# Kernel tuning notes

Hardware: AMD Instinct MI355X
Metric: run time of the kernel (lower is better)

Reference implementation:

```python
import jax, jax.numpy as jnp
import numpy as np

NUM_BINS = 16
D_MODEL = 128
TAIL_BOUND = 20.0
MIN_BIN_WIDTH = 1e-3
MIN_BIN_HEIGHT = 1e-3
MIN_DERIVATIVE = 1e-3
EPS = 1e-6


def setup_inputs() -> dict:
    key = jax.random.key(0)
    ks = jax.random.split(key, 10)
    B, S = 32, 8192
    sc = 0.05  # small init scale so spline logits stay moderate
    return {
        "inputs": jax.random.normal(ks[0], (B, S), dtype=jnp.float32),
        "conditioning": jax.random.normal(ks[1], (B, S, D_MODEL), dtype=jnp.float32),
        "Ww": jax.random.normal(ks[2], (NUM_BINS, D_MODEL), dtype=jnp.float32) * sc,
        "bw": jax.random.normal(ks[3], (NUM_BINS,), dtype=jnp.float32) * sc,
        "Wh": jax.random.normal(ks[4], (NUM_BINS, D_MODEL), dtype=jnp.float32) * sc,
        "bh": jax.random.normal(ks[5], (NUM_BINS,), dtype=jnp.float32) * sc,
        "Wd": jax.random.normal(ks[6], (NUM_BINS - 1, D_MODEL), dtype=jnp.float32) * sc,
        "bd": jax.random.normal(ks[7], (NUM_BINS - 1,), dtype=jnp.float32) * sc,
        "Wl": jax.random.normal(ks[8], (NUM_BINS, D_MODEL), dtype=jnp.float32) * sc,
        "bl": jax.random.normal(ks[9], (NUM_BINS,), dtype=jnp.float32) * sc,
    }


def _rational_linear_spline(x, uw, uh, ud, ul, left, right, bottom, top):
    nb = uw.shape[-1]
    # bin widths / cumulative widths
    w = MIN_BIN_WIDTH + (1.0 - MIN_BIN_WIDTH * nb) * jax.nn.softmax(uw, axis=-1)
    cw = jnp.concatenate([jnp.zeros_like(w[..., :1]), jnp.cumsum(w, axis=-1)], axis=-1)
    cw = (right - left) * cw + left
    cw = cw.at[..., 0].set(left).at[..., -1].set(right)
    w = cw[..., 1:] - cw[..., :-1]
    # derivatives (ud already padded to nb+1 by caller)
    d = MIN_DERIVATIVE + jax.nn.softplus(ud)
    # bin heights / cumulative heights
    h = MIN_BIN_HEIGHT + (1.0 - MIN_BIN_HEIGHT * nb) * jax.nn.softmax(uh, axis=-1)
    ch = jnp.concatenate([jnp.zeros_like(h[..., :1]), jnp.cumsum(h, axis=-1)], axis=-1)
    ch = (top - bottom) * ch + bottom
    ch = ch.at[..., 0].set(bottom).at[..., -1].set(top)
    h = ch[..., 1:] - ch[..., :-1]
    # searchsorted via sum of comparisons (as in source)
    locs = cw.at[..., -1].add(EPS)
    idx = jnp.sum((x[..., None] >= locs).astype(jnp.int32), axis=-1) - 1
    idx = jnp.clip(idx, 0, nb - 1)
    g = lambda t: jnp.take_along_axis(t, idx[..., None], axis=-1)[..., 0]
    in_cw = g(cw)
    in_bw = g(w)
    in_ch = g(ch)
    in_delta = g(h / w)
    dk = g(d)
    dk1 = g(d[..., 1:])
    in_h = g(h)
    lambdas = 0.95 * jax.nn.sigmoid(ul) + 0.025
    lam = g(lambdas)
    wa = 1.0
    wb = jnp.sqrt(dk / dk1) * wa
    wc = (lam * wa * dk + (1.0 - lam) * wb * dk1) / in_delta
    ya = in_ch
    yb = in_h + in_ch
    yc = ((1.0 - lam) * wa * ya + lam * wb * yb) / ((1.0 - lam) * wa + lam * wb)
    theta = (x - in_cw) / in_bw
    m = theta <= lam
    num = jnp.where(m, wa * ya * (lam - theta) + wc * yc * theta,
                    wc * yc * (1.0 - theta) + wb * yb * (theta - lam))
    den = jnp.where(m, wa * (lam - theta) + wc * theta,
                    wc * (1.0 - theta) + wb * (theta - lam))
    out = num / den
    deriv_num = jnp.where(m, wa * wc * lam * (yc - ya), wb * wc * (1.0 - lam) * (yb - yc)) / in_bw
    logabsdet = jnp.log(deriv_num) - 2.0 * jnp.log(jnp.abs(den))
    return out, logabsdet


def reference(inputs, conditioning, Ww, bw, Wh, bh, Wd, bd, Wl, bl):
    # parameter nets (module.forward): note the module normalizes here AND the
    # spline normalizes again -- replicate faithfully.
    uw = jax.nn.softmax(jnp.einsum('bsd,kd->bsk', conditioning, Ww) + bw, axis=-1)
    uh = jax.nn.softmax(jnp.einsum('bsd,kd->bsk', conditioning, Wh) + bh, axis=-1)
    ud = jax.nn.softplus(jnp.einsum('bsd,kd->bsk', conditioning, Wd) + bd)
    ul = jax.nn.sigmoid(jnp.einsum('bsd,kd->bsk', conditioning, Wl) + bl)
    # linear tails: pad derivatives with constant so boundary derivative == 1
    const = float(np.log(np.exp(1.0 - MIN_DERIVATIVE) - 1.0))
    edge = jnp.full(ud.shape[:-1] + (1,), const, dtype=ud.dtype)
    udp = jnp.concatenate([edge, ud, edge], axis=-1)  # [B,S,nb+1]
    tb = TAIL_BOUND
    inside = (inputs >= -tb) & (inputs <= tb)
    xc = jnp.clip(inputs, -tb, tb)
    s_out, s_lad = _rational_linear_spline(xc, uw, uh, udp, ul, -tb, tb, -tb, tb)
    outputs = jnp.where(inside, s_out, inputs)
    logabsdet = jnp.where(inside, s_lad, 0.0)
    return outputs, logabsdet
```

## Files before the change

kernel.cpp:

```cpp
#include <hip/hip_runtime.h>
#include <math.h>

#define NB 16
#define DM 128
#define BM 256
#define ZSTRIDE 68

typedef _Float16 half8  __attribute__((ext_vector_type(8)));
typedef _Float16 half4v __attribute__((ext_vector_type(4)));
typedef _Float16 half2v __attribute__((ext_vector_type(2)));
typedef __fp16   fp16x2 __attribute__((ext_vector_type(2)));
typedef float    f32x4  __attribute__((ext_vector_type(4)));

__device__ __forceinline__ float frcp_(float x) { return __builtin_amdgcn_rcpf(x); }
__device__ __forceinline__ float softplus_fast(float x) {
    return fmaxf(x, 0.0f) + __logf(1.0f + __expf(-fabsf(x)));
}
__device__ __forceinline__ float sigmoid_fast(float x) {
    return frcp_(1.0f + __expf(-x));
}
__device__ __forceinline__ void softmax16_m(float* z) {
    float m = z[0];
#pragma unroll
    for (int k = 1; k < NB; k++) m = fmaxf(m, z[k]);
    float s = 0.0f;
#pragma unroll
    for (int k = 0; k < NB; k++) { z[k] = __expf(z[k] - m); s += z[k]; }
    float r = frcp_(s);
#pragma unroll
    for (int k = 0; k < NB; k++) z[k] *= r;
}
__device__ __forceinline__ void softmax16_nm(float* z) {
    float s = 0.0f;
#pragma unroll
    for (int k = 0; k < NB; k++) { z[k] = __expf(z[k]); s += z[k]; }
    float r = frcp_(s);
#pragma unroll
    for (int k = 0; k < NB; k++) z[k] *= r;
}

__device__ __forceinline__ half2v pk_(float lo, float hi) {
    fp16x2 p = __builtin_amdgcn_cvt_pkrtz(lo, hi);
    return __builtin_bit_cast(half2v, p);
}
__device__ __forceinline__ half8 cvt8(float4 a0, float4 a1) {
    half2v p0 = pk_(a0.x, a0.y);
    half2v p1 = pk_(a0.z, a0.w);
    half2v p2 = pk_(a1.x, a1.y);
    half2v p3 = pk_(a1.z, a1.w);
    half8 f;
    f[0] = p0[0]; f[1] = p0[1]; f[2] = p1[0]; f[3] = p1[1];
    f[4] = p2[0]; f[5] = p2[1]; f[6] = p3[0]; f[7] = p3[1];
    return f;
}

#define LOADC(P, cr)                                    \
    P##0 = *(const float4*)((cr) + 0);                  \
    P##1 = *(const float4*)((cr) + 16);                 \
    P##2 = *(const float4*)((cr) + 32);                 \
    P##3 = *(const float4*)((cr) + 48);                 \
    P##4 = *(const float4*)((cr) + 64);                 \
    P##5 = *(const float4*)((cr) + 80);                 \
    P##6 = *(const float4*)((cr) + 96);                 \
    P##7 = *(const float4*)((cr) + 112);

#define CVTC(P)                                         \
    af0 = cvt8(P##0, P##1);                             \
    af1 = cvt8(P##2, P##3);                             \
    af2 = cvt8(P##4, P##5);                             \
    af3 = cvt8(P##6, P##7);

#define MFMA_GRP(af, s) {                                                       \
    const half8 bt0 = *(const half8*)(Blds + (((0*4+(s))*64 + lane) * 8));      \
    const half8 bt1 = *(const half8*)(Blds + (((1*4+(s))*64 + lane) * 8));      \
    const half8 bt2 = *(const half8*)(Blds + (((2*4+(s))*64 + lane) * 8));      \
    const half8 bt3 = *(const half8*)(Blds + (((3*4+(s))*64 + lane) * 8));      \
    acc0 = __builtin_amdgcn_mfma_f32_16x16x32_f16(af, bt0, acc0, 0, 0, 0);      \
    acc1 = __builtin_amdgcn_mfma_f32_16x16x32_f16(af, bt1, acc1, 0, 0, 0);      \
    acc2 = __builtin_amdgcn_mfma_f32_16x16x32_f16(af, bt2, acc2, 0, 0, 0);      \
    acc3 = __builtin_amdgcn_mfma_f32_16x16x32_f16(af, bt3, acc3, 0, 0, 0);      \
}

#define STOREZ(c) {                                                             \
    _Float16* zpw = zbase + (size_t)((c) * 16) * ZSTRIDE;                       \
    _Pragma("unroll")                                                           \
    for (int r = 0; r < 4; r++) {                                               \
        half2v p0 = pk_(acc0[r], acc1[r]);                                      \
        half2v p1 = pk_(acc2[r], acc3[r]);                                      \
        half4v w; w[0] = p0[0]; w[1] = p0[1]; w[2] = p1[0]; w[3] = p1[1];       \
        *(half4v*)(zpw + (size_t)r * ZSTRIDE) = w;                              \
    } }

#define RESET_ACC  acc0 = zf4; acc1 = zf4; acc2 = zf4; acc3 = zf4;

#define GEMM_CHUNK(P, c)                                                        \
    CVTC(P)                                                                     \
    MFMA_GRP(af0, 0) MFMA_GRP(af1, 1) MFMA_GRP(af2, 2) MFMA_GRP(af3, 3)         \
    STOREZ(c) RESET_ACC

#define STAGE_B_LDS(Wt, isWd) {                                                 \
    const bool val = (!(isWd)) || (l15 < 15);                                   \
    const float* srcl = (Wt) + (size_t)(val ? l15 : 0) * DM + lg * 4;           \
    float4 q0 = *(const float4*)(srcl + 0),  q1 = *(const float4*)(srcl + 16);  \
    float4 q2 = *(const float4*)(srcl + 32), q3 = *(const float4*)(srcl + 48);  \
    float4 q4 = *(const float4*)(srcl + 64), q5 = *(const float4*)(srcl + 80);  \
    float4 q6 = *(const float4*)(srcl + 96), q7 = *(const float4*)(srcl + 112); \
    half8 Q0 = val ? cvt8(q0, q1) : hz;                                         \
    half8 Q1 = val ? cvt8(q2, q3) : hz;                                         \
    half8 Q2 = val ? cvt8(q4, q5) : hz;                                         \
    half8 Q3 = val ? cvt8(q6, q7) : hz;                                         \
    *(half8*)(Blds + (((wave*4+0)*64 + lane) * 8)) = Q0;                        \
    *(half8*)(Blds + (((wave*4+1)*64 + lane) * 8)) = Q1;                        \
    *(half8*)(Blds + (((wave*4+2)*64 + lane) * 8)) = Q2;                        \
    *(half8*)(Blds + (((wave*4+3)*64 + lane) * 8)) = Q3;                        \
}

#define FENCE_LDS                                       \
    __builtin_amdgcn_sched_barrier(0);                  \
    asm volatile("s_waitcnt lgkmcnt(0)" ::: "memory");  \
    __builtin_amdgcn_sched_barrier(0);

#define CPTR(c) (cond + (((bRow + (size_t)(wave * 64 + (c) * 16 + l15)) < (size_t)N) \
                    ? (bRow + (size_t)(wave * 64 + (c) * 16 + l15))                  \
                    : ((size_t)N - 1)) * DM + lg * 4)

#define EPILOGUE(xv, giv)                                                        \
  if ((giv) < (size_t)N) {                                                       \
    float zw[NB], zh[NB], zl[NB], zd[NB - 1];                                    \
    const half4v* zr4 = (const half4v*)&Z[(size_t)tid * ZSTRIDE];                \
    _Pragma("unroll")                                                            \
    for (int j = 0; j < NB; j++) {                                               \
        half4v v = zr4[j];                                                       \
        zw[j] = (float)v[0] + bw[j];                                             \
        zh[j] = (float)v[1] + bh[j];                                             \
        zl[j] = (float)v[2] + bl[j];                                             \
        if (j < NB - 1) zd[j] = (float)v[3] + bd[j];                             \
    }                                                                            \
    float xc = fminf(fmaxf((xv), -20.0f), 20.0f);                                \
    softmax16_m(zw);                                                             \
    softmax16_nm(zw);                                                            \
    const float scale = (1.0f - 1e-3f * NB);                                     \
    float cw[NB + 1];                                                            \
    cw[0] = -20.0f;                                                              \
    float cum = 0.0f;                                                            \
    _Pragma("unroll")                                                            \
    for (int k = 0; k < NB; k++) {                                               \
        cum += 1e-3f + scale * zw[k];                                            \
        cw[k + 1] = 40.0f * cum - 20.0f;                                         \
    }                                                                            \
    cw[NB] = 20.0f;                                                              \
    softmax16_m(zh);                                                             \
    softmax16_nm(zh);                                                            \
    float ch[NB + 1];                                                            \
    ch[0] = -20.0f;                                                              \
    cum = 0.0f;                                                                  \
    _Pragma("unroll")                                                            \
    for (int k = 0; k < NB; k++) {                                               \
        cum += 1e-3f + scale * zh[k];                                            \
        ch[k + 1] = 40.0f * cum - 20.0f;                                         \
    }                                                                            \
    ch[NB] = 20.0f;                                                              \
    float in_cw = cw[0], cw_hi = cw[1], in_ch = ch[0], ch_hi = ch[1];            \
    float zl_sel = zl[0], zd_lo = zd[0], zd_hi = zd[0];                          \
    _Pragma("unroll")                                                            \
    for (int k = 1; k < NB; k++) {                                               \
        bool take = (xc >= cw[k]);                                               \
        in_cw  = take ? cw[k]     : in_cw;                                       \
        cw_hi  = take ? cw[k + 1] : cw_hi;                                       \
        in_ch  = take ? ch[k]     : in_ch;                                       \
        ch_hi  = take ? ch[k + 1] : ch_hi;                                       \
        zl_sel = take ? zl[k]     : zl_sel;                                      \
        zd_lo  = take ? zd[k - 1] : zd_lo;                                       \
        zd_hi  = take ? zd[(k < NB - 1) ? k : NB - 2] : zd_hi;                   \
    }                                                                            \
    bool firstbin = (xc <  cw[1]);                                               \
    bool lastbin  = (xc >= cw[NB - 1]);                                          \
    float in_bw = cw_hi - in_cw;                                                 \
    float in_h  = ch_hi - in_ch;                                                 \
    float dk  = firstbin ? 1.0f : (1e-3f + softplus_fast(softplus_fast(zd_lo))); \
    float dk1 = lastbin  ? 1.0f : (1e-3f + softplus_fast(softplus_fast(zd_hi))); \
    float ul  = sigmoid_fast(zl_sel);                                            \
    float lam = 0.95f * sigmoid_fast(ul) + 0.025f;                               \
    float rbw = frcp_(in_bw);                                                    \
    float in_delta = in_h * rbw;                                                 \
    float wb = sqrtf(dk * frcp_(dk1));                                           \
    float wc = (lam * dk + (1.0f - lam) * wb * dk1) * frcp_(in_delta);           \
    float ya = in_ch;                                                            \
    float yb = in_h + in_ch;                                                     \
    float yc = ((1.0f - lam) * ya + lam * wb * yb) * frcp_((1.0f - lam) + lam * wb); \
    float theta = (xc - in_cw) * rbw;                                            \
    bool mlt = (theta <= lam);                                                   \
    float num = mlt ? (ya * (lam - theta) + wc * yc * theta)                     \
                    : (wc * yc * (1.0f - theta) + wb * yb * (theta - lam));      \
    float den = mlt ? ((lam - theta) + wc * theta)                               \
                    : (wc * (1.0f - theta) + wb * (theta - lam));                \
    float sout = num * frcp_(den);                                               \
    float dnum = (mlt ? (wc * lam * (yc - ya))                                   \
                      : (wb * wc * (1.0f - lam) * (yb - yc))) * rbw;             \
    float slad = __logf(dnum) - 2.0f * __logf(fabsf(den));                       \
    bool inside = ((xv) >= -20.0f) && ((xv) <= 20.0f);                           \
    out[(giv)] = inside ? sout : (xv);                                           \
    lad[(giv)] = inside ? slad : 0.0f;                                           \
  }

__global__ __launch_bounds__(256, 3) void spline_mfma(
    const float* __restrict__ xin, const float* __restrict__ cond,
    const float* __restrict__ Ww, const float* __restrict__ bw,
    const float* __restrict__ Wh, const float* __restrict__ bh,
    const float* __restrict__ Wd, const float* __restrict__ bd,
    const float* __restrict__ Wl, const float* __restrict__ bl,
    float* __restrict__ out, float* __restrict__ lad, int N)
{
    __shared__ __align__(16) _Float16 Z[BM * ZSTRIDE];
    __shared__ __align__(16) _Float16 Blds[16 * 64 * 8];

    const int tid  = threadIdx.x;
    const int wave = tid >> 6;
    const int lane = tid & 63;
    const int l15  = lane & 15;
    const int lg   = lane >> 4;

    const size_t bRow = (size_t)blockIdx.x * BM;
    const size_t gi = bRow + tid;

    half8 hz;
    hz[0]=hz[1]=hz[2]=hz[3]=hz[4]=hz[5]=hz[6]=hz[7] = (_Float16)0.0f;
    {
        const float* Wt = (wave == 0) ? Ww : (wave == 1) ? Wh : (wave == 2) ? Wl : Wd;
        const bool isWd = (wave == 3);
        STAGE_B_LDS(Wt, isWd)
    }
    __syncthreads();

    float4 X0, X1, X2, X3, X4, X5, X6, X7;
    float4 Y0, Y1, Y2, Y3, Y4, Y5, Y6, Y7;
    LOADC(X, CPTR(0))
    LOADC(Y, CPTR(1))
    float x = xin[gi < (size_t)N ? gi : 0];

    const f32x4 zf4 = {0.f, 0.f, 0.f, 0.f};
    f32x4 acc0 = zf4, acc1 = zf4, acc2 = zf4, acc3 = zf4;
    half8 af0, af1, af2, af3;
    _Float16* zbase = &Z[(size_t)(wave * 64 + lg * 4) * ZSTRIDE + l15 * 4];

    GEMM_CHUNK(X, 0)
    LOADC(X, CPTR(2))
    GEMM_CHUNK(Y, 1)
    LOADC(Y, CPTR(3))
    GEMM_CHUNK(X, 2)
    GEMM_CHUNK(Y, 3)

    FENCE_LDS
    EPILOGUE(x, gi)
}

extern "C" void kernel_launch(void* const* d_in, const int* in_sizes, int n_in,
                              void* d_out, int out_size, void* d_ws, size_t ws_size,
                              hipStream_t stream) {
    const float* xin  = (const float*)d_in[0];
    const float* cond = (const float*)d_in[1];
    const float* Ww   = (const float*)d_in[2];
    const float* bwp  = (const float*)d_in[3];
    const float* Wh   = (const float*)d_in[4];
    const float* bhp  = (const float*)d_in[5];
    const float* Wd   = (const float*)d_in[6];
    const float* bdp  = (const float*)d_in[7];
    const float* Wl   = (const float*)d_in[8];
    const float* blp  = (const float*)d_in[9];
    int N = in_sizes[0];
    float* out = (float*)d_out;
    float* lad = out + N;
    int grid = (N + BM - 1) / BM;
    hipLaunchKernelGGL(spline_mfma, dim3(grid), dim3(256), 0, stream,
                       xin, cond, Ww, bwp, Wh, bhp, Wd, bdp, Wl, blp, out, lad, N);
}
```

Baseline: 33.84 us.

## Grow blocks to 1024 threads and stream cumulative bin edges in epilogue

```diff
diff --git a/kernel.cpp b/kernel.cpp
--- a/kernel.cpp
+++ b/kernel.cpp
@@ -3,7 +3,7 @@
 
 #define NB 16
 #define DM 128
-#define BM 256
+#define BM 1024
 #define ZSTRIDE 68
 
 typedef _Float16 half8  __attribute__((ext_vector_type(8)));
@@ -137,44 +137,35 @@
         if (j < NB - 1) zd[j] = (float)v[3] + bd[j];                             \
     }                                                                            \
     float xc = fminf(fmaxf((xv), -20.0f), 20.0f);                                \
-    softmax16_m(zw);                                                             \
-    softmax16_nm(zw);                                                            \
+    softmax16_m(zw); softmax16_nm(zw);                                           \
+    softmax16_m(zh); softmax16_nm(zh);                                           \
     const float scale = (1.0f - 1e-3f * NB);                                     \
-    float cw[NB + 1];                                                            \
-    cw[0] = -20.0f;                                                              \
-    float cum = 0.0f;                                                            \
-    _Pragma("unroll")                                                            \
-    for (int k = 0; k < NB; k++) {                                               \
-        cum += 1e-3f + scale * zw[k];                                            \
-        cw[k + 1] = 40.0f * cum - 20.0f;                                         \
-    }                                                                            \
-    cw[NB] = 20.0f;                                                              \
-    softmax16_m(zh);                                                             \
-    softmax16_nm(zh);                                                            \
-    float ch[NB + 1];                                                            \
-    ch[0] = -20.0f;                                                              \
-    cum = 0.0f;                                                                  \
-    _Pragma("unroll")                                                            \
-    for (int k = 0; k < NB; k++) {                                               \
-        cum += 1e-3f + scale * zh[k];                                            \
-        ch[k + 1] = 40.0f * cum - 20.0f;                                         \
-    }                                                                            \
-    ch[NB] = 20.0f;                                                              \
-    float in_cw = cw[0], cw_hi = cw[1], in_ch = ch[0], ch_hi = ch[1];            \
+    float cum_w = 1e-3f + scale * zw[0];                                         \
+    float cum_h = 1e-3f + scale * zh[0];                                         \
+    float cw_k1 = 40.0f * cum_w - 20.0f;                              \
+    float ch_k1 = 40.0f * cum_h - 20.0f;                                         \
+    const float cw1 = cw_k1;                                                     \
+    float in_cw = -20.0f, cw_hi = cw_k1, in_ch = -20.0f, ch_hi = ch_k1;          \
     float zl_sel = zl[0], zd_lo = zd[0], zd_hi = zd[0];                          \
+    bool lastbin = false;                                                        \
     _Pragma("unroll")                                                            \
     for (int k = 1; k < NB; k++) {                                               \
-        bool take = (xc >= cw[k]);                                               \
-        in_cw  = take ? cw[k]     : in_cw;                                       \
-        cw_hi  = take ? cw[k + 1] : cw_hi;                                       \
-        in_ch  = take ? ch[k]     : in_ch;                                       \
-        ch_hi  = take ? ch[k + 1] : ch_hi;                                       \
-        zl_sel = take ? zl[k]     : zl_sel;                                      \
+        cum_w += 1e-3f + scale * zw[k];                                          \
+        cum_h += 1e-3f + scale * zh[k];                                          \
+        float cw_k2 = (k == NB - 1) ? 20.0f : (40.0f * cum_w - 20.0f);           \
+        float ch_k2 = (k == NB - 1) ? 20.0f : (40.0f * cum_h - 20.0f);           \
+        bool take = (xc >= cw_k1);                              \
+        in_cw  = take ? cw_k1 : in_cw;                                           \
+        cw_hi  = take ? cw_k2 : cw_hi;                                           \
+        in_ch  = take ? ch_k1 : in_ch;                                           \
+        ch_hi  = take ? ch_k2 : ch_hi;                                           \
+        zl_sel = take ? zl[k] : zl_sel;                                          \
         zd_lo  = take ? zd[k - 1] : zd_lo;                                       \
         zd_hi  = take ? zd[(k < NB - 1) ? k : NB - 2] : zd_hi;                   \
+        if (k == NB - 1) lastbin = take;                                         \
+        cw_k1 = cw_k2; ch_k1 = ch_k2;                                            \
     }                                                                            \
-    bool firstbin = (xc <  cw[1]);                                               \
-    bool lastbin  = (xc >= cw[NB - 1]);                                          \
+    bool firstbin = (xc < cw1);                                                  \
     float in_bw = cw_hi - in_cw;                                                 \
     float in_h  = ch_hi - in_ch;                                                 \
     float dk  = firstbin ? 1.0f : (1e-3f + softplus_fast(softplus_fast(zd_lo))); \
@@ -203,7 +194,7 @@
     lad[(giv)] = inside ? slad : 0.0f;                                           \
   }
 
-__global__ __launch_bounds__(256, 3) void spline_mfma(
+__global__ __launch_bounds__(1024, 4) void spline_mfma(
     const float* __restrict__ xin, const float* __restrict__ cond,
     const float* __restrict__ Ww, const float* __restrict__ bw,
     const float* __restrict__ Wh, const float* __restrict__ bh,
@@ -225,7 +216,7 @@
 
     half8 hz;
     hz[0]=hz[1]=hz[2]=hz[3]=hz[4]=hz[5]=hz[6]=hz[7] = (_Float16)0.0f;
-    {
+    if (wave < 4) {
         const float* Wt = (wave == 0) ? Ww : (wave == 1) ? Wh : (wave == 2) ? Wl : Wd;
         const bool isWd = (wave == 3);
         STAGE_B_LDS(Wt, isWd)
@@ -271,6 +262,6 @@
     float* out = (float*)d_out;
     float* lad = out + N;
     int grid = (N + BM - 1) / BM;
-    hipLaunchKernelGGL(spline_mfma, dim3(grid), dim3(256), 0, stream,
+    hipLaunchKernelGGL(spline_mfma, dim3(grid), dim3(1024), 0, stream,
                        xin, cond, Ww, bwp, Wh, bhp, Wd, bdp, Wl, blp, out, lad, N);
 }
```

Measured after the change: 52.76 us. 1.56x slower.
